# Performance work log

Hardware: AMD Instinct MI355X
Metric: run time of the kernel (lower is better)

Reference implementation:

```python
import jax, jax.numpy as jnp
import numpy as np

L, H, D, T, DFF, OUT, B = 6, 12, 49, 16, 1024, 10, 8192
STD = 0.02


def setup_inputs() -> dict:
    key = jax.random.key(0)
    ks = jax.random.split(key, 24)
    n = lambda k, shape: jax.random.normal(k, shape, dtype=jnp.float32) * STD
    return {
        "x": jax.random.normal(ks[0], (B, 784), dtype=jnp.float32),
        "mask": jnp.ones((B, T), dtype=bool),  # unused by the original Attention
        # per-layer, per-head Q/K/V/out linears (weights stored as (in, out))
        "Wq": n(ks[1], (L, H, D, D)), "bq": n(ks[2], (L, H, D)),
        "Wk": n(ks[3], (L, H, D, D)), "bk": n(ks[4], (L, H, D)),
        "Wv": n(ks[5], (L, H, D, D)), "bv": n(ks[6], (L, H, D)),
        "Wo": n(ks[7], (L, H, D, D)), "bo": n(ks[8], (L, H, D)),
        # concat projection Linear(D*H, D)
        "Wcat": n(ks[9], (L, H * D, D)), "bcat": n(ks[10], (L, D)),
        # LayerNorms
        "ln1_g": jnp.ones((L, D), jnp.float32), "ln1_b": jnp.zeros((L, D), jnp.float32),
        "ln2_g": jnp.ones((L, D), jnp.float32), "ln2_b": jnp.zeros((L, D), jnp.float32),
        # FeedForward
        "W1": n(ks[11], (L, D, DFF)), "b1": n(ks[12], (L, DFF)),
        "W2": n(ks[13], (L, DFF, D)), "b2": n(ks[14], (L, D)),
        # ClassificationHead
        "Wc": n(ks[15], (D, OUT)), "bc": n(ks[16], (OUT,)),
    }


def _ln(x, g, b):
    mu = jnp.mean(x, axis=-1, keepdims=True)
    var = jnp.mean((x - mu) ** 2, axis=-1, keepdims=True)
    return (x - mu) / jnp.sqrt(var + 1e-5) * g + b


def _forward(x, Wq, bq, Wk, bk, Wv, bv, Wo, bo, Wcat, bcat,
             ln1_g, ln1_b, ln2_g, ln2_b, W1, b1, W2, b2, Wc, bc):
    bsz = x.shape[0]
    h = x.reshape(bsz, T, D)  # MakeTokens
    scale = float(1.0 / np.sqrt(D))
    for i in range(L):
        xn = _ln(h, ln1_g[i], ln1_b[i])
        # all heads batched via einsum (each head attends over full d_model)
        q = jnp.einsum('btd,hde->bhte', xn, Wq[i]) + bq[i][None, :, None, :]
        k = jnp.einsum('btd,hde->bhte', xn, Wk[i]) + bk[i][None, :, None, :]
        v = jnp.einsum('btd,hde->bhte', xn, Wv[i]) + bv[i][None, :, None, :]
        w = jax.nn.softmax(jnp.einsum('bhte,bhse->bhts', q, k) * scale, axis=-1)
        o = jnp.einsum('bhts,bhse->bhte', w, v)
        o = jnp.einsum('bhte,hef->bhtf', o, Wo[i]) + bo[i][None, :, None, :]
        cat = o.transpose(0, 2, 1, 3).reshape(bsz, T, H * D)  # concat heads
        attn = cat @ Wcat[i] + bcat[i]
        x2 = h + attn  # dropout is identity at inference
        xn2 = _ln(x2, ln2_g[i], ln2_b[i])
        ff = jax.nn.relu(xn2 @ W1[i] + b1[i]) @ W2[i] + b2[i]
        h = x2 + ff
    return h[:, 0, :] @ Wc + bc  # ClassificationHead on token 0


def reference(x, mask, Wq, bq, Wk, bk, Wv, bv, Wo, bo, Wcat, bcat,
              ln1_g, ln1_b, ln2_g, ln2_b, W1, b1, W2, b2, Wc, bc):
    # mask is accepted but unused, matching the original Attention.forward
    return _forward(x, Wq, bq, Wk, bk, Wv, bv, Wo, bo, Wcat, bcat,
                    ln1_g, ln1_b, ln2_g, ln2_b, W1, b1, W2, b2, Wc, bc)
```

## Files before the change

kernel.cpp:

```cpp
#include <hip/hip_runtime.h>
#include <hip/hip_bf16.h>

#define LYR 6
#define NH 12
#define DM 49
#define FFD 1024
#define NOUT 10
#define NB 8192
#define NWIN 204
#define SPW 2

typedef __bf16 bf16x8 __attribute__((ext_vector_type(8)));
typedef float f32x4 __attribute__((ext_vector_type(4)));
typedef unsigned int u32;
typedef u32 u32x4 __attribute__((ext_vector_type(4)));

static __device__ __forceinline__ f32x4 mfma_full(u32x4 a, u32x4 b, f32x4 c) {
  return __builtin_amdgcn_mfma_f32_16x16x32_bf16(
      __builtin_bit_cast(bf16x8, a), __builtin_bit_cast(bf16x8, b), c, 0, 0, 0);
}

static __device__ __forceinline__ f32x4 mfma_hz(u32 a0, u32 a1, u32 b0, u32 b1, f32x4 c) {
  u32x4 A = {a0, a1, 0u, 0u};
  u32x4 B = {b0, b1, 0u, 0u};
  return mfma_full(A, B, c);
}

static __device__ __forceinline__ unsigned short f2bf(float f) {
  union { float f; unsigned u; } c; c.f = f;
  unsigned r = c.u + 0x7fffu + ((c.u >> 16) & 1u);
  return (unsigned short)(r >> 16);
}

static __device__ __forceinline__ u32 pk2(float a, float b) {
  __hip_bfloat162 h2 = __float22bfloat162_rn(make_float2(a, b));
  u32 r;
  __builtin_memcpy(&r, &h2, 4);
  return r;
}

static __device__ __forceinline__ void gload16(const void* gp, void* lp) {
  __builtin_amdgcn_global_load_lds(
      (const __attribute__((address_space(1))) unsigned int*)gp,
      (__attribute__((address_space(3))) unsigned int*)lp, 16, 0, 0);
}

static __device__ __forceinline__ void decode(int idx, int& d, int& col) {
  int tile = idx >> 10, ks = (idx >> 9) & 1, lane = (idx >> 3) & 63, j = idx & 7;
  col = 16 * tile + (lane & 15);
  d = 16 * (2 * ks + (j >= 4 ? 1 : 0)) + 4 * (lane >> 4) + (j & 3);
}


__global__ void prep_g_frag(const float* __restrict__ Wq, const float* __restrict__ bq,
                            const float* __restrict__ Wk, const float* __restrict__ bk,
                            unsigned short* __restrict__ blob) {
  const float QS = 1.44269504088896f / 7.0f;
  int lh = blockIdx.x, l = lh / NH, hd = lh % NH;
  unsigned short* base =
      blob + (size_t)(l * 34 + 3 * (hd >> 1)) * 8192 + (hd & 1) * 4096;
  for (int idx = threadIdx.x; idx < 4096; idx += blockDim.x) {
    int kk, cc;
    decode(idx, kk, cc);
    float acc = 0.f;
    if (cc <= DM && kk <= DM) {
      for (int e = 0; e < DM; ++e) {
        float kv = (cc < DM) ? Wk[(size_t)lh * 2401 + cc * DM + e] : bk[lh * DM + e];
        float qv = (kk < DM) ? Wq[(size_t)lh * 2401 + kk * DM + e] : bq[lh * DM + e];
        acc += kv * qv;
      }
      acc *= QS;
    }
    base[idx] = f2bf(acc);
  }
}

__global__ void prep_v_frag(const float* __restrict__ Wv, const float* __restrict__ bv,
                            unsigned short* __restrict__ blob) {
  int lh = blockIdx.x, l = lh / NH, hd = lh % NH;
  unsigned short* base =
      blob + (size_t)(l * 34 + 3 * (hd >> 1) + 1 + (hd & 1)) * 8192;
  for (int idx = threadIdx.x; idx < 4096; idx += blockDim.x) {
    int d, e;
    decode(idx, d, e);
    float v = 0.f;
    if (e < DM) {
      if (d < DM) v = Wv[(size_t)lh * 2401 + d * DM + e];
      else if (d == DM) v = bv[lh * DM + e];
    }
    base[idx] = f2bf(v);
  }
}

__global__ void prep_comb_frag(const float* __restrict__ Wo, const float* __restrict__ bo,
                               const float* __restrict__ Wcat, const float* __restrict__ bcat,
                               unsigned short* __restrict__ blob) {
  int lh = blockIdx.x, l = lh / NH, hh = lh % NH;
  unsigned short* base =
      blob + (size_t)(l * 34 + 3 * (hh >> 1) + 1 + (hh & 1)) * 8192 + 4096;
  for (int idx = threadIdx.x; idx < 4096; idx += blockDim.x) {
    int e, f;
    decode(idx, e, f);
    float val = 0.f;
    if (f < DM) {
      if (e < DM) {
        for (int c = 0; c < DM; ++c)
          val += Wo[(size_t)lh * 2401 + e * DM + c] *
                 Wcat[((size_t)l * 588 + hh * DM + c) * DM + f];
      } else if (e == DM) {
        for (int c = 0; c < DM; ++c)
          val += bo[lh * DM + c] * Wcat[((size_t)l * 588 + hh * DM + c) * DM + f];
        if (hh == 0) val += bcat[l * DM + f];
      }
    }
    base[idx] = f2bf(val);
  }
}

__global__ void prep_ff_frag(const float* __restrict__ W1, const float* __restrict__ b1,
                             const float* __restrict__ W2,
                             unsigned short* __restrict__ blob) {
  int l = blockIdx.x >> 3, part = blockIdx.x & 7;
  for (int idx = part * 16384 + threadIdx.x; idx < (part + 1) * 16384; idx += blockDim.x) {
    int c = idx >> 13, within = idx & 8191, sec = within >> 12, sidx = within & 4095;
    unsigned short* dst =
        blob + (size_t)(l * 34 + 18 + c) * 8192 + sec * 4096;
    int d, col;
    decode(sidx, d, col);
    float v = 0.f;
    if (sec == 0) {
      int jcol = 64 * c + col;
      if (d < DM) v = W1[(size_t)l * DM * FFD + d * FFD + jcol];
      else if (d == DM) v = b1[l * FFD + jcol];
    } else {
      int jg = 64 * c + d;
      if (col < DM) v = W2[(size_t)l * FFD * DM + jg * DM + col];
    }
    dst[sidx] = f2bf(v);
  }
}

__global__ void prep_small(const float* __restrict__ g1, const float* __restrict__ b1,
                           const float* __restrict__ g2, const float* __restrict__ b2,
                           const float* __restrict__ bff2,
                           float* __restrict__ g1p, float* __restrict__ b1p,
                           float* __restrict__ g2p, float* __restrict__ b2p,
                           float* __restrict__ bff2p) {
  int idx = threadIdx.x;
  if (idx >= 384) return;
  int l = idx >> 6, d = idx & 63;
  bool v = d < DM;
  g1p[idx] = v ? g1[l * DM + d] : 0.f;
  b1p[idx] = v ? b1[l * DM + d] : 0.f;
  g2p[idx] = v ? g2[l * DM + d] : 0.f;
  b2p[idx] = v ? b2[l * DM + d] : 0.f;
  bff2p[idx] = v ? bff2[l * DM + d] : 0.f;
}


static __device__ __forceinline__ void ln_pack(const f32x4 (&h)[4], const f32x4 (&gv)[4],
                                               const f32x4 (&bv)[4], int g, u32x4 (&xf)[2]) {
  float s = 0.f, s2 = 0.f;
#pragma unroll
  for (int mi = 0; mi < 4; ++mi)
#pragma unroll
    for (int r = 0; r < 4; ++r) { float v = h[mi][r]; s += v; s2 += v * v; }
  s += __shfl_xor(s, 16, 64); s += __shfl_xor(s, 32, 64);
  s2 += __shfl_xor(s2, 16, 64); s2 += __shfl_xor(s2, 32, 64);
  float mu = s * (1.f / 49.f);
  float rs = rsqrtf(s2 * (1.f / 49.f) - mu * mu + 1e-5f);
  u32 t[8];
#pragma unroll
  for (int mi = 0; mi < 4; ++mi) {
    float xv[4];
#pragma unroll
    for (int r = 0; r < 4; ++r) xv[r] = (h[mi][r] - mu) * rs * gv[mi][r] + bv[mi][r];
    if (mi == 3) xv[1] = (g == 0) ? 1.0f : xv[1];
    t[2 * mi] = pk2(xv[0], xv[1]);
    t[2 * mi + 1] = pk2(xv[2], xv[3]);
  }
  xf[0] = u32x4{t[0], t[1], t[2], t[3]};
  xf[1] = u32x4{t[4], t[5], t[6], t[7]};
}

static __device__ __forceinline__ void softmax_pk(f32x4 s, u32& p0, u32& p1) {
  float e0 = exp2f(s[0]), e1 = exp2f(s[1]);
  float e2 = exp2f(s[2]), e3 = exp2f(s[3]);
  float su = e0 + e1 + e2 + e3;
  su += __shfl_xor(su, 16, 64);
  su += __shfl_xor(su, 32, 64);
  float inv = 1.f / su;
  p0 = pk2(e0 * inv, e1 * inv);
  p1 = pk2(e2 * inv, e3 * inv);
}

#define STAGE_LOAD(s)                                                         \
  do {                                                                        \
    const unsigned short* gsrc = blob + (size_t)(s) * 8192 + tid * 8;         \
    unsigned short* ldst = &wbuf[(s) & 1][wv * 512];                          \
    _Pragma("unroll") for (int r = 0; r < 4; ++r)                             \
        gload16(gsrc + r * 2048, ldst + r * 2048);                            \
  } while (0)

__global__ __launch_bounds__(256, 4) void transformer_kernel(
    const float* __restrict__ x, float* __restrict__ out,
    const unsigned short* __restrict__ blob,
    const float* __restrict__ lg1, const float* __restrict__ lb1,
    const float* __restrict__ lg2, const float* __restrict__ lb2,
    const float* __restrict__ b2p, const float* __restrict__ Wc,
    const float* __restrict__ bc) {
  __shared__ __align__(16) unsigned short wbuf[2][8192];
  const int tid = threadIdx.x;
  const int wv = tid >> 6, lane = tid & 63;
  const int g = lane >> 4, li = lane & 15;
  const int s0 = blockIdx.x * 8 + wv * 2;
  const f32x4 z4 = {0.f, 0.f, 0.f, 0.f};

  STAGE_LOAD(0);

  f32x4 h[SPW][4];
#pragma unroll
  for (int s = 0; s < SPW; ++s) {
    const float* xa = x + (size_t)(s0 + s) * 784 + li * DM;
#pragma unroll
    for (int mi = 0; mi < 4; ++mi)
#pragma unroll
      for (int r = 0; r < 4; ++r) {
        int d = 16 * mi + 4 * g + r;
        h[s][mi][r] = (d < DM) ? xa[d] : 0.f;
      }
  }

  int w = 0;
  for (int layer = 0; layer < LYR; ++layer) {
    u32x4 xf[SPW][2];
    {
      f32x4 gv[4], bv[4];
#pragma unroll
      for (int mi = 0; mi < 4; ++mi) {
        int off = layer * 64 + 16 * mi + 4 * g;
        gv[mi] = *(const f32x4*)(lg1 + off);
        bv[mi] = *(const f32x4*)(lb1 + off);
      }
#pragma unroll
      for (int s = 0; s < SPW; ++s) ln_pack(h[s], gv, bv, g, xf[s]);
    }

    for (int hp = 0; hp < 6; ++hp) {
      __syncthreads();
      if (w + 1 < NWIN) STAGE_LOAD(w + 1);
      u32 p[2][SPW][2];
#pragma unroll
      for (int hh = 0; hh < 2; ++hh) {
        const u32x4* GW = (const u32x4*)(wbuf[w & 1] + hh * 4096);
        __builtin_amdgcn_s_setprio(1);
        u32x4 yf[SPW][2];
#pragma unroll
        for (int mi = 0; mi < 4; ++mi) {
          f32x4 cy[SPW];
#pragma unroll
          for (int s = 0; s < SPW; ++s) cy[s] = z4;
#pragma unroll
          for (int ks = 0; ks < 2; ++ks) {
            u32x4 gw = GW[(mi * 2 + ks) * 64 + lane];
#pragma unroll
            for (int s = 0; s < SPW; ++s) cy[s] = mfma_full(gw, xf[s][ks], cy[s]);
          }
#pragma unroll
          for (int s = 0; s < SPW; ++s) {
            yf[s][mi >> 1][2 * (mi & 1)] = pk2(cy[s][0], cy[s][1]);
            yf[s][mi >> 1][2 * (mi & 1) + 1] = pk2(cy[s][2], cy[s][3]);
          }
        }
        f32x4 sc[SPW];
#pragma unroll
        for (int s = 0; s < SPW; ++s) {
          sc[s] = mfma_full(xf[s][0], yf[s][0], z4);
          sc[s] = mfma_full(xf[s][1], yf[s][1], sc[s]);
        }
        __builtin_amdgcn_s_setprio(0);
#pragma unroll
        for (int s = 0; s < SPW; ++s) softmax_pk(sc[s], p[hh][s][0], p[hh][s][1]);
      }
      ++w;

#pragma unroll
      for (int hh = 0; hh < 2; ++hh) {
        __syncthreads();
        if (w + 1 < NWIN) STAGE_LOAD(w + 1);
        const u32x4* VW = (const u32x4*)wbuf[w & 1];
        const u32x4* CW = (const u32x4*)(wbuf[w & 1] + 4096);
        __builtin_amdgcn_s_setprio(1);
        u32 vf_[SPW][4][2];
#pragma unroll
        for (int nt = 0; nt < 4; ++nt) {
          f32x4 cv[SPW];
#pragma unroll
          for (int s = 0; s < SPW; ++s) cv[s] = z4;
#pragma unroll
          for (int ks = 0; ks < 2; ++ks) {
            u32x4 wvv = VW[(nt * 2 + ks) * 64 + lane];
#pragma unroll
            for (int s = 0; s < SPW; ++s) cv[s] = mfma_full(xf[s][ks], wvv, cv[s]);
          }
#pragma unroll
          for (int s = 0; s < SPW; ++s) {
            vf_[s][nt][0] = pk2(cv[s][0], cv[s][1]);
            vf_[s][nt][1] = pk2(cv[s][2], cv[s][3]);
          }
        }
        u32x4 of_[SPW][2];
#pragma unroll
        for (int nt = 0; nt < 4; ++nt) {
#pragma unroll
          for (int s = 0; s < SPW; ++s) {
            f32x4 c = mfma_hz(vf_[s][nt][0], vf_[s][nt][1], p[hh][s][0], p[hh][s][1], z4);
            if (nt == 3) c[1] = (g == 0) ? 1.0f : c[1];
            of_[s][nt >> 1][2 * (nt & 1)] = pk2(c[0], c[1]);
            of_[s][nt >> 1][2 * (nt & 1) + 1] = pk2(c[2], c[3]);
          }
        }
#pragma unroll
        for (int ft = 0; ft < 4; ++ft) {
#pragma unroll
          for (int ks = 0; ks < 2; ++ks) {
            u32x4 wc = CW[(ft * 2 + ks) * 64 + lane];
#pragma unroll
            for (int s = 0; s < SPW; ++s) h[s][ft] = mfma_full(wc, of_[s][ks], h[s][ft]);
          }
        }
        __builtin_amdgcn_s_setprio(0);
        ++w;
      }
    }

    {
      f32x4 gv[4], bv[4];
#pragma unroll
      for (int mi = 0; mi < 4; ++mi) {
        int off = layer * 64 + 16 * mi + 4 * g;
        gv[mi] = *(const f32x4*)(lg2 + off);
        bv[mi] = *(const f32x4*)(lb2 + off);
      }
#pragma unroll
      for (int s = 0; s < SPW; ++s) ln_pack(h[s], gv, bv, g, xf[s]);
#pragma unroll
      for (int mi = 0; mi < 4; ++mi) {
        f32x4 bb = *(const f32x4*)(b2p + layer * 64 + 16 * mi + 4 * g);
#pragma unroll
        for (int s = 0; s < SPW; ++s) h[s][mi] += bb;
      }
    }

    for (int c = 0; c < 16; ++c) {
      __syncthreads();
      if (w + 1 < NWIN) STAGE_LOAD(w + 1);
      const u32x4* W1c = (const u32x4*)wbuf[w & 1];
      const u32x4* W2c = (const u32x4*)(wbuf[w & 1] + 4096);
      __builtin_amdgcn_s_setprio(1);
      u32x4 af[SPW][2];
#pragma unroll
      for (int jt = 0; jt < 4; ++jt) {
        f32x4 ca[SPW];
#pragma unroll
        for (int s = 0; s < SPW; ++s) ca[s] = z4;
#pragma unroll
        for (int ks = 0; ks < 2; ++ks) {
          u32x4 ww = W1c[(jt * 2 + ks) * 64 + lane];
#pragma unroll
          for (int s = 0; s < SPW; ++s) ca[s] = mfma_full(ww, xf[s][ks], ca[s]);
        }
#pragma unroll
        for (int s = 0; s < SPW; ++s) {
          float r0 = fmaxf(ca[s][0], 0.f), r1 = fmaxf(ca[s][1], 0.f);
          float r2 = fmaxf(ca[s][2], 0.f), r3 = fmaxf(ca[s][3], 0.f);
          af[s][jt >> 1][2 * (jt & 1)] = pk2(r0, r1);
          af[s][jt >> 1][2 * (jt & 1) + 1] = pk2(r2, r3);
        }
      }
#pragma unroll
      for (int ft = 0; ft < 4; ++ft) {
#pragma unroll
        for (int ks = 0; ks < 2; ++ks) {
          u32x4 ww = W2c[(ft * 2 + ks) * 64 + lane];
#pragma unroll
          for (int s = 0; s < SPW; ++s) h[s][ft] = mfma_full(ww, af[s][ks], h[s][ft]);
        }
      }
      __builtin_amdgcn_s_setprio(0);
      ++w;
    }
  }

  __syncthreads();
  float* hs = (float*)&wbuf[0][0];
  if (li == 0) {
#pragma unroll
    for (int s = 0; s < SPW; ++s)
#pragma unroll
      for (int mi = 0; mi < 4; ++mi)
#pragma unroll
        for (int r = 0; r < 4; ++r)
          hs[(wv * SPW + s) * 64 + 16 * mi + 4 * g + r] = h[s][mi][r];
  }
  __syncthreads();
  if (lane < 10 * SPW) {
    int smp = lane / 10, c = lane % 10;
    float acc = bc[c];
    const float* hrow = hs + (wv * SPW + smp) * 64;
    for (int d = 0; d < DM; ++d) acc += hrow[d] * Wc[d * NOUT + c];
    out[(size_t)(s0 + smp) * NOUT + c] = acc;
  }
}

extern "C" void kernel_launch(void* const* d_in, const int* in_sizes, int n_in,
                              void* d_out, int out_size, void* d_ws, size_t ws_size,
                              hipStream_t stream) {
  const float* x = (const float*)d_in[0];
  const float* Wq = (const float*)d_in[2];
  const float* bq = (const float*)d_in[3];
  const float* Wk = (const float*)d_in[4];
  const float* bk = (const float*)d_in[5];
  const float* Wv = (const float*)d_in[6];
  const float* bv = (const float*)d_in[7];
  const float* Wo = (const float*)d_in[8];
  const float* bo = (const float*)d_in[9];
  const float* Wcat = (const float*)d_in[10];
  const float* bcat = (const float*)d_in[11];
  const float* ln1_g = (const float*)d_in[12];
  const float* ln1_b = (const float*)d_in[13];
  const float* ln2_g = (const float*)d_in[14];
  const float* ln2_b = (const float*)d_in[15];
  const float* W1 = (const float*)d_in[16];
  const float* b1 = (const float*)d_in[17];
  const float* W2 = (const float*)d_in[18];
  const float* b2 = (const float*)d_in[19];
  const float* Wc = (const float*)d_in[20];
  const float* bc = (const float*)d_in[21];

  unsigned short* blob = (unsigned short*)d_ws;
  float* fp = (float*)(blob + (size_t)NWIN * 8192);
  float* g1p = fp;
  float* b1p = g1p + 384;
  float* g2p = b1p + 384;
  float* b2lp = g2p + 384;
  float* b2p = b2lp + 384;

  prep_g_frag<<<72, 256, 0, stream>>>(Wq, bq, Wk, bk, blob);
  prep_v_frag<<<72, 256, 0, stream>>>(Wv, bv, blob);
  prep_comb_frag<<<72, 256, 0, stream>>>(Wo, bo, Wcat, bcat, blob);
  prep_ff_frag<<<48, 256, 0, stream>>>(W1, b1, W2, blob);
  prep_small<<<1, 384, 0, stream>>>(ln1_g, ln1_b, ln2_g, ln2_b, b2, g1p, b1p, g2p, b2lp, b2p);

  transformer_kernel<<<NB / 8, 256, 0, stream>>>(
      x, (float*)d_out, blob, g1p, b1p, g2p, b2lp, b2p, Wc, bc);
}
```

Measured before the change: 580.8 us.

## Fold value and output projections into one per-head matrix applied before attention

Precomputes the product of Wv with the combined Wo·Wcat matrix per head, including the bias rows, so the main kernel projects tokens once and multiplies by the softmax weights, accumulating straight into the residual. This drops one MFMA stage and one weight window per head pair, cutting the streamed weight blob from 34 to 28 windows per layer and removing one barrier per head pair. The fold relies on softmax rows summing to one so the bias terms carry through. The extra bf16 rounding of the combined matrix may slightly change numerics.

```diff
diff --git a/kernel.cpp b/kernel.cpp
--- a/kernel.cpp
+++ b/kernel.cpp
@@ -7,7 +7,7 @@
 #define FFD 1024
 #define NOUT 10
 #define NB 8192
-#define NWIN 204
+#define NWIN 168
 #define SPW 2
 
 typedef __bf16 bf16x8 __attribute__((ext_vector_type(8)));
@@ -58,7 +58,7 @@
   const float QS = 1.44269504088896f / 7.0f;
   int lh = blockIdx.x, l = lh / NH, hd = lh % NH;
   unsigned short* base =
-      blob + (size_t)(l * 34 + 3 * (hd >> 1)) * 8192 + (hd & 1) * 4096;
+      blob + (size_t)(l * 28 + 2 * (hd >> 1)) * 8192 + (hd & 1) * 4096;
   for (int idx = threadIdx.x; idx < 4096; idx += blockDim.x) {
     int kk, cc;
     decode(idx, kk, cc);
@@ -75,45 +75,48 @@
   }
 }
 
-__global__ void prep_v_frag(const float* __restrict__ Wv, const float* __restrict__ bv,
-                            unsigned short* __restrict__ blob) {
-  int lh = blockIdx.x, l = lh / NH, hd = lh % NH;
-  unsigned short* base =
-      blob + (size_t)(l * 34 + 3 * (hd >> 1) + 1 + (hd & 1)) * 8192;
-  for (int idx = threadIdx.x; idx < 4096; idx += blockDim.x) {
-    int d, e;
-    decode(idx, d, e);
-    float v = 0.f;
-    if (e < DM) {
-      if (d < DM) v = Wv[(size_t)lh * 2401 + d * DM + e];
-      else if (d == DM) v = bv[lh * DM + e];
-    }
-    base[idx] = f2bf(v);
-  }
-}
-
-__global__ void prep_comb_frag(const float* __restrict__ Wo, const float* __restrict__ bo,
-                               const float* __restrict__ Wcat, const float* __restrict__ bcat,
-                               unsigned short* __restrict__ blob) {
+__global__ void prep_comb_f32(const float* __restrict__ Wo, const float* __restrict__ bo,
+                              const float* __restrict__ Wcat, const float* __restrict__ bcat,
+                              float* __restrict__ C) {
   int lh = blockIdx.x, l = lh / NH, hh = lh % NH;
-  unsigned short* base =
-      blob + (size_t)(l * 34 + 3 * (hh >> 1) + 1 + (hh & 1)) * 8192 + 4096;
-  for (int idx = threadIdx.x; idx < 4096; idx += blockDim.x) {
-    int e, f;
-    decode(idx, e, f);
+  float* base = C + (size_t)lh * 3200;
+  for (int idx = threadIdx.x; idx < 3200; idx += blockDim.x) {
+    int e = idx >> 6, f = idx & 63;
     float val = 0.f;
     if (f < DM) {
       if (e < DM) {
         for (int c = 0; c < DM; ++c)
           val += Wo[(size_t)lh * 2401 + e * DM + c] *
                  Wcat[((size_t)l * 588 + hh * DM + c) * DM + f];
-      } else if (e == DM) {
+      } else {
         for (int c = 0; c < DM; ++c)
           val += bo[lh * DM + c] * Wcat[((size_t)l * 588 + hh * DM + c) * DM + f];
         if (hh == 0) val += bcat[l * DM + f];
       }
     }
-    base[idx] = f2bf(val);
+    base[idx] = val;
+  }
+}
+
+__global__ void prep_vc_frag(const float* __restrict__ Wv, const float* __restrict__ bv,
+                             const float* __restrict__ C,
+                             unsigned short* __restrict__ blob) {
+  int lh = blockIdx.x, l = lh / NH, hd = lh % NH;
+  const float* Cb = C + (size_t)lh * 3200;
+  unsigned short* base =
+      blob + (size_t)(l * 28 + 2 * (hd >> 1) + 1) * 8192 + (hd & 1) * 4096;
+  for (int idx = threadIdx.x; idx < 4096; idx += blockDim.x) {
+    int d, f;
+    decode(idx, d, f);
+    float acc = 0.f;
+    if (f < DM && d <= DM) {
+      for (int e = 0; e < DM; ++e) {
+        float wv = (d < DM) ? Wv[(size_t)lh * 2401 + d * DM + e] : bv[lh * DM + e];
+        acc += wv * Cb[e * 64 + f];
+      }
+      if (d == DM) acc += Cb[DM * 64 + f];
+    }
+    base[idx] = f2bf(acc);
   }
 }
 
@@ -124,7 +127,7 @@
   for (int idx = part * 16384 + threadIdx.x; idx < (part + 1) * 16384; idx += blockDim.x) {
     int c = idx >> 13, within = idx & 8191, sec = within >> 12, sidx = within & 4095;
     unsigned short* dst =
-        blob + (size_t)(l * 34 + 18 + c) * 8192 + sec * 4096;
+        blob + (size_t)(l * 28 + 12 + c) * 8192 + sec * 4096;
     int d, col;
     decode(sidx, d, col);
     float v = 0.f;
@@ -284,54 +287,33 @@
       }
       ++w;
 
+      __syncthreads();
+      if (w + 1 < NWIN) STAGE_LOAD(w + 1);
 #pragma unroll
       for (int hh = 0; hh < 2; ++hh) {
-        __syncthreads();
-        if (w + 1 < NWIN) STAGE_LOAD(w + 1);
-        const u32x4* VW = (const u32x4*)wbuf[w & 1];
-        const u32x4* CW = (const u32x4*)(wbuf[w & 1] + 4096);
+        const u32x4* UW = (const u32x4*)(wbuf[w & 1] + hh * 4096);
         __builtin_amdgcn_s_setprio(1);
-        u32 vf_[SPW][4][2];
 #pragma unroll
         for (int nt = 0; nt < 4; ++nt) {
-          f32x4 cv[SPW];
-#pragma unroll
-          for (int s = 0; s < SPW; ++s) cv[s] = z4;
+          f32x4 cu[SPW];
+#pragma unroll
+          for (int s = 0; s < SPW; ++s) cu[s] = z4;
 #pragma unroll
           for (int ks = 0; ks < 2; ++ks) {
-            u32x4 wvv = VW[(nt * 2 + ks) * 64 + lane];
-#pragma unroll
-            for (int s = 0; s < SPW; ++s) cv[s] = mfma_full(xf[s][ks], wvv, cv[s]);
+            u32x4 wu = UW[(nt * 2 + ks) * 64 + lane];
+#pragma unroll
+            for (int s = 0; s < SPW; ++s) cu[s] = mfma_full(xf[s][ks], wu, cu[s]);
           }
 #pragma unroll
           for (int s = 0; s < SPW; ++s) {
-            vf_[s][nt][0] = pk2(cv[s][0], cv[s][1]);
-            vf_[s][nt][1] = pk2(cv[s][2], cv[s][3]);
+            u32 u0 = pk2(cu[s][0], cu[s][1]);
+            u32 u1 = pk2(cu[s][2], cu[s][3]);
+            h[s][nt] = mfma_hz(u0, u1, p[hh][s][0], p[hh][s][1], h[s][nt]);
           }
         }
-        u32x4 of_[SPW][2];
-#pragma unroll
-        for (int nt = 0; nt < 4; ++nt) {
-#pragma unroll
-          for (int s = 0; s < SPW; ++s) {
-            f32x4 c = mfma_hz(vf_[s][nt][0], vf_[s][nt][1], p[hh][s][0], p[hh][s][1], z4);
-            if (nt == 3) c[1] = (g == 0) ? 1.0f : c[1];
-            of_[s][nt >> 1][2 * (nt & 1)] = pk2(c[0], c[1]);
-            of_[s][nt >> 1][2 * (nt & 1) + 1] = pk2(c[2], c[3]);
-          }
-        }
-#pragma unroll
-        for (int ft = 0; ft < 4; ++ft) {
-#pragma unroll
-          for (int ks = 0; ks < 2; ++ks) {
-            u32x4 wc = CW[(ft * 2 + ks) * 64 + lane];
-#pragma unroll
-            for (int s = 0; s < SPW; ++s) h[s][ft] = mfma_full(wc, of_[s][ks], h[s][ft]);
-          }
-        }
         __builtin_amdgcn_s_setprio(0);
-        ++w;
-      }
+      }
+      ++w;
     }
 
     {
@@ -439,7 +421,8 @@
   const float* bc = (const float*)d_in[21];
 
   unsigned short* blob = (unsigned short*)d_ws;
-  float* fp = (float*)(blob + (size_t)NWIN * 8192);
+  float* Cscr = (float*)(blob + (size_t)NWIN * 8192);
+  float* fp = Cscr + (size_t)72 * 3200;
   float* g1p = fp;
   float* b1p = g1p + 384;
   float* g2p = b1p + 384;
@@ -447,8 +430,8 @@
   float* b2p = b2lp + 384;
 
   prep_g_frag<<<72, 256, 0, stream>>>(Wq, bq, Wk, bk, blob);
-  prep_v_frag<<<72, 256, 0, stream>>>(Wv, bv, blob);
-  prep_comb_frag<<<72, 256, 0, stream>>>(Wo, bo, Wcat, bcat, blob);
+  prep_comb_f32<<<72, 256, 0, stream>>>(Wo, bo, Wcat, bcat, Cscr);
+  prep_vc_frag<<<72, 256, 0, stream>>>(Wv, bv, Cscr, blob);
   prep_ff_frag<<<48, 256, 0, stream>>>(W1, b1, W2, blob);
   prep_small<<<1, 384, 0, stream>>>(ln1_g, ln1_b, ln2_g, ln2_b, b2, g1p, b1p, g2p, b2lp, b2p);
 
```

Result: faster. 526.1 us (-9.4%).
